# Performance work log

Hardware: AMD Instinct MI355X
Metric: run time of the kernel (lower is better)

## Reference

```python
import jax, jax.numpy as jnp
import numpy as np

NUM_HEADS = 32
NUM_KV_HEADS = 8
HEAD_DIM = 128
HIDDEN = 4096
RANK = 8
ALPHA = 16.0
SCALING = ALPHA / RANK
EPS = 1e-8


def dora_linear(x, W, A, B, m):
    # DoRA: W_eff = W + scaling * B @ A; directional component normalized per
    # output row, rescaled by learned magnitude m.
    W_eff = W + SCALING * (B @ A)                      # [out, in]
    norm = jnp.linalg.norm(W_eff, axis=1)              # [out]
    W_d = W_eff * (m / (norm + EPS))[:, None]
    return x @ W_d.T


def setup_inputs() -> dict:
    key = jax.random.key(0)
    ks = jax.random.split(key, 16)
    B_, S = 2, 2048
    hidden_states = jax.random.normal(ks[0], (B_, S, HIDDEN), jnp.float32)
    # additive causal mask
    causal = jnp.triu(jnp.full((S, S), -1e9, jnp.float32), k=1)
    attention_mask = jnp.broadcast_to(causal, (B_, 1, S, S))

    def w(k, shape, scale=0.02):
        return scale * jax.random.normal(k, shape, jnp.float32)

    Wq = w(ks[1], (HIDDEN, HIDDEN)); Aq = w(ks[2], (RANK, HIDDEN)); Bq = w(ks[3], (HIDDEN, RANK))
    Wk = w(ks[4], (NUM_KV_HEADS * HEAD_DIM, HIDDEN)); Ak = w(ks[5], (RANK, HIDDEN)); Bk = w(ks[6], (NUM_KV_HEADS * HEAD_DIM, RANK))
    Wv = w(ks[7], (NUM_KV_HEADS * HEAD_DIM, HIDDEN)); Av = w(ks[8], (RANK, HIDDEN)); Bv = w(ks[9], (NUM_KV_HEADS * HEAD_DIM, RANK))
    Wo = w(ks[10], (HIDDEN, HIDDEN)); Ao = w(ks[11], (RANK, HIDDEN)); Bo = w(ks[12], (HIDDEN, RANK))
    # DoRA magnitude init: column-norm of base weight (per output row)
    mq = jnp.linalg.norm(Wq, axis=1)
    mk = jnp.linalg.norm(Wk, axis=1)
    mv = jnp.linalg.norm(Wv, axis=1)
    mo = jnp.linalg.norm(Wo, axis=1)
    return dict(hidden_states=hidden_states, attention_mask=attention_mask,
                Wq=Wq, Aq=Aq, Bq=Bq, mq=mq,
                Wk=Wk, Ak=Ak, Bk=Bk, mk=mk,
                Wv=Wv, Av=Av, Bv=Bv, mv=mv,
                Wo=Wo, Ao=Ao, Bo=Bo, mo=mo)


def reference(hidden_states, attention_mask,
              Wq, Aq, Bq, mq, Wk, Ak, Bk, mk,
              Wv, Av, Bv, mv, Wo, Ao, Bo, mo):
    bsz, q_len, _ = hidden_states.shape
    n_rep = NUM_HEADS // NUM_KV_HEADS

    q = dora_linear(hidden_states, Wq, Aq, Bq, mq)
    k = dora_linear(hidden_states, Wk, Ak, Bk, mk)
    v = dora_linear(hidden_states, Wv, Av, Bv, mv)

    q = q.reshape(bsz, q_len, NUM_HEADS, HEAD_DIM).transpose(0, 2, 1, 3)
    k = k.reshape(bsz, q_len, NUM_KV_HEADS, HEAD_DIM).transpose(0, 2, 1, 3)
    v = v.reshape(bsz, q_len, NUM_KV_HEADS, HEAD_DIM).transpose(0, 2, 1, 3)

    # _apply_rotary_pos_emb is a no-op in the source: (q, k) unchanged

    # repeat_kv for grouped-query attention
    k = jnp.repeat(k, n_rep, axis=1)  # [b, H, s, d]
    v = jnp.repeat(v, n_rep, axis=1)

    scale = 1.0 / jnp.sqrt(jnp.float32(HEAD_DIM))
    attn_weights = jnp.einsum('bhqd,bhkd->bhqk', q, k) * scale
    attn_weights = attn_weights + attention_mask
    attn_weights = jax.nn.softmax(attn_weights, axis=-1)
    attn_output = jnp.einsum('bhqk,bhkd->bhqd', attn_weights, v)
    attn_output = attn_output.transpose(0, 2, 1, 3).reshape(bsz, q_len, HIDDEN)
    attn_output = dora_linear(attn_output, Wo, Ao, Bo, mo)
    return attn_output
```

## Files before the change

### kernel.cpp

```cpp
#include <hip/hip_runtime.h>
#include <hip/hip_bf16.h>
#include <stdint.h>

#define HIDDEN 4096
#define RANK   8
#define SCALING 2.0f
#define EPS    1e-8f
#define SEQ    2048
#define BATCH  2
#define NH     32
#define NKVH   8
#define HD     128
#define MROWS  (BATCH*SEQ)
#define NQKV   6144

typedef __attribute__((ext_vector_type(8))) short bf16x8;
typedef __attribute__((ext_vector_type(4))) short bf16x4;
typedef __attribute__((ext_vector_type(4))) float f32x4;

__device__ __forceinline__ void gload_lds16(const void* g, void* lds) {
  __builtin_amdgcn_global_load_lds((__attribute__((address_space(1))) void*)g,
                                   (__attribute__((address_space(3))) void*)lds,
                                   16, 0, 0);
}

__device__ __forceinline__ unsigned short f2bf(float f) {
  __hip_bfloat16 h = __float2bfloat16(f);
  return *reinterpret_cast<unsigned short*>(&h);
}

__device__ __forceinline__ void store_c(float* p, float v) { *p = v; }
__device__ __forceinline__ void store_c(__hip_bfloat16* p, float v) { *p = __float2bfloat16(v); }

__device__ __forceinline__ bf16x8 lds_read8_b64(const short* p) {
  bf16x4 lo = *(const bf16x4*)p;
  bf16x4 hi = *(const bf16x4*)(p + 4);
  bf16x8 r;
  r[0]=lo[0]; r[1]=lo[1]; r[2]=lo[2]; r[3]=lo[3];
  r[4]=hi[0]; r[5]=hi[1]; r[6]=hi[2]; r[7]=hi[3];
  return r;
}

__device__ __forceinline__ void wd_row(const float* __restrict__ W, const float* __restrict__ A,
                                       const float* __restrict__ B, const float* __restrict__ m,
                                       unsigned short* __restrict__ out, int row, int tid,
                                       float* wsum) {
  float bl[RANK];
#pragma unroll
  for (int t = 0; t < RANK; ++t) bl[t] = SCALING * B[row*RANK + t];
  float ev[16];
  float ss = 0.f;
#pragma unroll
  for (int it = 0; it < 4; ++it) {
    const int j = it*1024 + tid*4;
    const float4 wv = *(const float4*)&W[(size_t)row*HIDDEN + j];
    float e0 = wv.x, e1 = wv.y, e2 = wv.z, e3 = wv.w;
#pragma unroll
    for (int t = 0; t < RANK; ++t) {
      const float4 av = *(const float4*)&A[t*HIDDEN + j];
      e0 += bl[t]*av.x; e1 += bl[t]*av.y; e2 += bl[t]*av.z; e3 += bl[t]*av.w;
    }
    ev[it*4+0]=e0; ev[it*4+1]=e1; ev[it*4+2]=e2; ev[it*4+3]=e3;
    ss += e0*e0 + e1*e1 + e2*e2 + e3*e3;
  }
#pragma unroll
  for (int off = 32; off > 0; off >>= 1) ss += __shfl_down(ss, off, 64);
  if ((tid & 63) == 0) wsum[tid >> 6] = ss;
  __syncthreads();
  const float norm = sqrtf(wsum[0]+wsum[1]+wsum[2]+wsum[3]);
  const float scl = m[row] / (norm + EPS);
#pragma unroll
  for (int it = 0; it < 4; ++it) {
    const int j = it*1024 + tid*4;
    ushort4 pk;
    pk.x = f2bf(ev[it*4+0]*scl); pk.y = f2bf(ev[it*4+1]*scl);
    pk.z = f2bf(ev[it*4+2]*scl); pk.w = f2bf(ev[it*4+3]*scl);
    *(ushort4*)&out[(size_t)row*HIDDEN + j] = pk;
  }
}

__launch_bounds__(256)
__global__ void prep_kernel(const float* __restrict__ x, unsigned short* __restrict__ xbf,
                            const float* Wq, const float* Aq, const float* Bq, const float* mq, unsigned short* wdq,
                            const float* Wk, const float* Ak, const float* Bk, const float* mk, unsigned short* wdk,
                            const float* Wv, const float* Av, const float* Bv, const float* mv, unsigned short* wdv,
                            const float* Wo, const float* Ao, const float* Bo, const float* mo, unsigned short* wdo) {
  __shared__ float wsum[4];
  const int bid = blockIdx.x;
  const int tid = threadIdx.x;
  if (bid < 16384) {
    const size_t i = ((size_t)bid * 256 + tid) * 4;
    const float4 v = *(const float4*)&x[i];
    ushort4 pk;
    pk.x = f2bf(v.x); pk.y = f2bf(v.y); pk.z = f2bf(v.z); pk.w = f2bf(v.w);
    *(ushort4*)&xbf[i] = pk;
  } else if (bid < 20480) {
    wd_row(Wq, Aq, Bq, mq, wdq, bid - 16384, tid, wsum);
  } else if (bid < 21504) {
    wd_row(Wk, Ak, Bk, mk, wdk, bid - 20480, tid, wsum);
  } else if (bid < 22528) {
    wd_row(Wv, Av, Bv, mv, wdv, bid - 21504, tid, wsum);
  } else {
    wd_row(Wo, Ao, Bo, mo, wdo, bid - 22528, tid, wsum);
  }
}

__launch_bounds__(256)
__global__ void wd_kernel(const float* __restrict__ W, const float* __restrict__ A,
                          const float* __restrict__ B, const float* __restrict__ m,
                          unsigned short* __restrict__ out) {
  __shared__ float wsum[4];
  wd_row(W, A, B, m, out, blockIdx.x, threadIdx.x, wsum);
}

__device__ __forceinline__ void stage_unit(const __hip_bfloat16* __restrict__ Ab,
                                           const __hip_bfloat16* __restrict__ Bb,
                                           const int K, __hip_bfloat16* sbuf,
                                           const int tau, const int j,
                                           const int w, const int l, const int kchunk) {
  const __hip_bfloat16* src = (j & 1) ? Bb : Ab;
  __hip_bfloat16* dst = sbuf + ((tau & 1) << 15) + (j << 13);
  const int k0 = (tau << 6) + ((j >> 1) << 5) + (kchunk << 3);
  const int r0 = (w << 4) + (l >> 2);
  gload_lds16(src + (size_t)r0 * K + k0, dst + (w << 9));
  gload_lds16(src + (size_t)(r0 + 128) * K + k0, dst + 4096 + (w << 9));
}

template<typename CT, int NREP>
__launch_bounds__(512, 2)
__global__ void gemm256(const __hip_bfloat16* __restrict__ A,
                        const __hip_bfloat16* __restrict__ B,
                        CT* __restrict__ C, const int M, const int N, const int K) {
  (void)M;
  __shared__ __hip_bfloat16 sb[65536];
  const int tid = threadIdx.x;
  const int w = tid >> 6, l = tid & 63;
  const int wr = w >> 2, wc = w & 3;
  const int q4 = l >> 4, ln = l & 15;
  const int nbn = N / (NREP * 64);
  const int cpx = gridDim.x >> 3;
  const int fid = (blockIdx.x & 7) * cpx + (blockIdx.x >> 3);
  const int tM = (fid / nbn) << 8;
  const int tN = (fid % nbn) * (NREP * 64);
  const int NT = K >> 6;
  const __hip_bfloat16* Ab = A + (size_t)tM * K;
  const __hip_bfloat16* Bb = B + (size_t)tN * K;
  const int kchunk = (l & 3) ^ ((l >> 3) & 3);
  const int slotoff = (q4 ^ ((ln >> 1) & 3)) << 3;

  f32x4 acc[8][NREP] = {};
  bf16x8 bfr[NREP] = {};

#pragma unroll
  for (int s = 0; s < 6; ++s)
    stage_unit(Ab, Bb, K, sb, s >> 2, s & 3, w, l, kchunk);
  asm volatile("s_waitcnt vmcnt(4)" ::: "memory");
  __builtin_amdgcn_s_barrier();

  for (int tt = 0; tt < NT; tt += 2) {
#pragma unroll
    for (int hlf = 0; hlf < 2; ++hlf) {
      const int t_ = tt + hlf;
      const short* base = (const short*)sb + (hlf << 15);
#pragma unroll
      for (int q = 0; q < 4; ++q) {
        const int ks = q >> 1;
        const int mh = q & 1;
        bf16x8 af[4];
        const short* Au = base + (ks << 14);
#pragma unroll
        for (int i = 0; i < 4; ++i) {
          const int row = wr * 128 + (mh * 4 + i) * 16 + ln;
          af[i] = *(const bf16x8*)&Au[row * 32 + slotoff];
        }
        if (mh == 0) {
          const short* Bu = base + 8192 + (ks << 14);
#pragma unroll
          for (int i = 0; i < NREP; ++i) {
            const int row = wc * (NREP * 16) + i * 16 + ln;
            bfr[i] = *(const bf16x8*)&Bu[row * 32 + slotoff];
          }
        }
        const int s = 4 * t_ + 6 + q;
        if ((s >> 2) < NT)
          stage_unit(Ab, Bb, K, sb, s >> 2, s & 3, w, l, kchunk);
        __builtin_amdgcn_s_barrier();
        __builtin_amdgcn_s_setprio(1);
#pragma unroll
        for (int i = 0; i < 4; ++i)
#pragma unroll
          for (int ni = 0; ni < NREP; ++ni)
            acc[mh * 4 + i][ni] = __builtin_amdgcn_mfma_f32_16x16x32_bf16(af[i], bfr[ni], acc[mh * 4 + i][ni], 0, 0, 0);
        __builtin_amdgcn_s_setprio(0);
        if (q == 3 && t_ < NT - 1) {
          if (t_ == NT - 2) asm volatile("s_waitcnt vmcnt(0)" ::: "memory");
          else              asm volatile("s_waitcnt vmcnt(4)" ::: "memory");
        }
        __builtin_amdgcn_s_barrier();
      }
    }
  }

  const int r0 = tM + wr * 128 + q4 * 4;
  const int c0 = tN + wc * (NREP * 16) + ln;
#pragma unroll
  for (int mi = 0; mi < 8; ++mi)
#pragma unroll
    for (int ni = 0; ni < NREP; ++ni)
#pragma unroll
      for (int r = 0; r < 4; ++r)
        store_c(&C[(size_t)(r0 + mi * 16 + r) * N + c0 + ni * 16], acc[mi][ni][r]);
}

#define VT_S 68
#define PS_S 68
__launch_bounds__(256, 3)
__global__ void attn_kernel(const __hip_bfloat16* __restrict__ qkv,
                            __hip_bfloat16* __restrict__ out) {
  const int bid = blockIdx.x;
  const int qt = 15 - (bid >> 6);
  const int hb = bid & 63;
  const int h  = hb & 31;
  const int b  = hb >> 5;
  const int kvh = h >> 2;
  const int tid = threadIdx.x;
  const int w = tid >> 6, l = tid & 63;
  const int q4 = l >> 4;
  const int ln = l & 15;
  const int sw = ln & 7;

  __shared__ __hip_bfloat16 Ks[64*128];
  __shared__ __hip_bfloat16 Vt[128*VT_S];
  __shared__ __hip_bfloat16 Ps[4][2][16*PS_S];

  const __hip_bfloat16* kb = qkv + (size_t)(b*SEQ)*NQKV + HIDDEN + kvh*HD;
  const __hip_bfloat16* vb = qkv + (size_t)(b*SEQ)*NQKV + (HIDDEN+1024) + kvh*HD;

  const int Q0 = qt*128;

  const int krow = l >> 4;
  const int kchunk = ((l & 15) ^ krow ^ ((w & 1) << 2)) * 8;

  const int vc4 = (tid & 15) * 4;
  const int vd0 = (tid >> 4) * 8;

  bf16x8 aq[2][4];
#pragma unroll
  for (int hf = 0; hf < 2; ++hf) {
    const __hip_bfloat16* qr = qkv + (size_t)(b*SEQ + Q0 + hf*64 + w*16 + ln)*NQKV + h*HD;
#pragma unroll
    for (int ks = 0; ks < 4; ++ks) {
      uint4 raw = *(const uint4*)(qr + ks*32 + q4*8);
      aq[hf][ks] = *(const bf16x8*)&raw;
    }
  }

  f32x4 o[2][8] = {};
  float mx[2] = {-1e30f, -1e30f};
  float lsum[2] = {0.f, 0.f};
  const float sc = 0.08838834764831845f;
  const int qabs0 = Q0 + w*16 + ln;

  const int jmax = 2*qt + 1;
  for (int j = 0; j <= jmax; ++j) {
    const int do0 = (j <= 2*qt);
    __syncthreads();
#pragma unroll
    for (int i = 0; i < 4; ++i) {
      const int rr = i*16 + w*4;
      gload_lds16(kb + (size_t)(j*64 + rr + krow)*NQKV + kchunk, &Ks[rr*128]);
    }
    {
      uint4 r0 = *(const uint4*)(vb + (size_t)(j*64 + vc4 + 0)*NQKV + vd0);
      uint4 r1 = *(const uint4*)(vb + (size_t)(j*64 + vc4 + 1)*NQKV + vd0);
      uint4 r2 = *(const uint4*)(vb + (size_t)(j*64 + vc4 + 2)*NQKV + vd0);
      uint4 r3 = *(const uint4*)(vb + (size_t)(j*64 + vc4 + 3)*NQKV + vd0);
      const unsigned short* p0 = (const unsigned short*)&r0;
      const unsigned short* p1 = (const unsigned short*)&r1;
      const unsigned short* p2 = (const unsigned short*)&r2;
      const unsigned short* p3 = (const unsigned short*)&r3;
#pragma unroll
      for (int t = 0; t < 8; ++t) {
        ushort4 pk; pk.x = p0[t]; pk.y = p1[t]; pk.z = p2[t]; pk.w = p3[t];
        *(ushort4*)&Vt[(vd0 + t)*VT_S + vc4] = pk;
      }
    }
    __syncthreads();

    f32x4 s[2][4] = {};
    const short* Kp = (const short*)Ks;
#pragma unroll
    for (int ks = 0; ks < 4; ++ks) {
      const int slot = ((ks*4 + q4) ^ sw) * 8;
#pragma unroll
      for (int nt = 0; nt < 4; ++nt) {
        bf16x8 bk = *(const bf16x8*)&Kp[(nt*16 + ln)*128 + slot];
        if (do0) s[0][nt] = __builtin_amdgcn_mfma_f32_16x16x32_bf16(bk, aq[0][ks], s[0][nt], 0, 0, 0);
        s[1][nt] = __builtin_amdgcn_mfma_f32_16x16x32_bf16(bk, aq[1][ks], s[1][nt], 0, 0, 0);
      }
    }

#pragma unroll
    for (int hf = 0; hf < 2; ++hf) {
      if (hf == 0 && !do0) continue;
      const int qabs = qabs0 + hf*64;
      if (j == 2*qt + hf) {
#pragma unroll
        for (int nt = 0; nt < 4; ++nt)
#pragma unroll
          for (int r = 0; r < 4; ++r) {
            const int kvabs = j*64 + nt*16 + q4*4 + r;
            if (kvabs > qabs) s[hf][nt][r] = -1e30f;
          }
      }
      float vmax = mx[hf];
#pragma unroll
      for (int nt = 0; nt < 4; ++nt)
#pragma unroll
        for (int r = 0; r < 4; ++r) vmax = fmaxf(vmax, s[hf][nt][r]);
      vmax = fmaxf(vmax, __shfl_xor(vmax, 16, 64));
      vmax = fmaxf(vmax, __shfl_xor(vmax, 32, 64));
      const float alpha = __expf((mx[hf] - vmax) * sc);
      float rs = 0.f;
#pragma unroll
      for (int nt = 0; nt < 4; ++nt)
#pragma unroll
        for (int r = 0; r < 4; ++r) {
          const float e = __expf((s[hf][nt][r] - vmax) * sc);
          s[hf][nt][r] = e; rs += e;
        }
      rs += __shfl_xor(rs, 16, 64);
      rs += __shfl_xor(rs, 32, 64);
      mx[hf] = vmax;
      lsum[hf] = lsum[hf]*alpha + rs;
#pragma unroll
      for (int r = 0; r < 4; ++r) {
        const float ar = __shfl(alpha, q4*4 + r, 64);
#pragma unroll
        for (int ni = 0; ni < 8; ++ni) o[hf][ni][r] *= ar;
      }
      __hip_bfloat16* Pw = Ps[w][hf];
#pragma unroll
      for (int nt = 0; nt < 4; ++nt) {
        ushort4 pk;
        pk.x = f2bf(s[hf][nt][0]); pk.y = f2bf(s[hf][nt][1]);
        pk.z = f2bf(s[hf][nt][2]); pk.w = f2bf(s[hf][nt][3]);
        *(ushort4*)&Pw[ln*PS_S + nt*16 + q4*4] = pk;
      }
    }

    const short* Vp = (const short*)Vt;
    const short* Pp0 = (const short*)Ps[w][0];
    const short* Pp1 = (const short*)Ps[w][1];
#pragma unroll
    for (int ks = 0; ks < 2; ++ks) {
      bf16x8 ap0 = lds_read8_b64(&Pp0[ln*PS_S + ks*32 + q4*8]);
      bf16x8 ap1 = lds_read8_b64(&Pp1[ln*PS_S + ks*32 + q4*8]);
#pragma unroll
      for (int ni = 0; ni < 8; ++ni) {
        bf16x8 bv = lds_read8_b64(&Vp[(ni*16 + ln)*VT_S + ks*32 + q4*8]);
        if (do0) o[0][ni] = __builtin_amdgcn_mfma_f32_16x16x32_bf16(ap0, bv, o[0][ni], 0, 0, 0);
        o[1][ni] = __builtin_amdgcn_mfma_f32_16x16x32_bf16(ap1, bv, o[1][ni], 0, 0, 0);
      }
    }
  }

#pragma unroll
  for (int hf = 0; hf < 2; ++hf) {
    const int row0 = b*SEQ + Q0 + hf*64 + w*16 + q4*4;
#pragma unroll
    for (int r = 0; r < 4; ++r) {
      const float lr = __shfl(lsum[hf], q4*4 + r, 64);
      const float inv = 1.f / lr;
#pragma unroll
      for (int ni = 0; ni < 8; ++ni)
        out[(size_t)(row0 + r)*HIDDEN + h*HD + ni*16 + ln] = __float2bfloat16(o[hf][ni][r] * inv);
    }
  }
}

extern "C" void kernel_launch(void* const* d_in, const int* in_sizes, int n_in,
                              void* d_out, int out_size, void* d_ws, size_t ws_size,
                              hipStream_t stream) {
  (void)in_sizes; (void)n_in; (void)out_size;
  const float* x  = (const float*)d_in[0];
  const float* Wq = (const float*)d_in[2];
  const float* Aq = (const float*)d_in[3];
  const float* Bq = (const float*)d_in[4];
  const float* mq = (const float*)d_in[5];
  const float* Wk = (const float*)d_in[6];
  const float* Ak = (const float*)d_in[7];
  const float* Bk = (const float*)d_in[8];
  const float* mk = (const float*)d_in[9];
  const float* Wv = (const float*)d_in[10];
  const float* Av = (const float*)d_in[11];
  const float* Bv = (const float*)d_in[12];
  const float* mv = (const float*)d_in[13];
  const float* Wo = (const float*)d_in[14];
  const float* Ao = (const float*)d_in[15];
  const float* Bo = (const float*)d_in[16];
  const float* mo = (const float*)d_in[17];

  char* ws = (char*)d_ws;
  __hip_bfloat16* xbf = (__hip_bfloat16*)ws;
  __hip_bfloat16* wd  = (__hip_bfloat16*)(ws + (size_t)33554432);
  __hip_bfloat16* qkv = (__hip_bfloat16*)(ws + (size_t)83886080);
  const bool big = ws_size >= (size_t)167772160;
  __hip_bfloat16* wdo = big ? (__hip_bfloat16*)(ws + (size_t)134217728) : wd;

  prep_kernel<<<big ? 26624 : 22528, 256, 0, stream>>>(
      x, (unsigned short*)xbf,
      Wq, Aq, Bq, mq, (unsigned short*)wd,
      Wk, Ak, Bk, mk, (unsigned short*)(wd + (size_t)4096*4096),
      Wv, Av, Bv, mv, (unsigned short*)(wd + (size_t)5120*4096),
      Wo, Ao, Bo, mo, (unsigned short*)wdo);
  gemm256<__hip_bfloat16, 3><<<512, 512, 0, stream>>>(xbf, wd, qkv, MROWS, NQKV, HIDDEN);
  if (!big)
    wd_kernel<<<4096, 256, 0, stream>>>(Wo, Ao, Bo, mo, (unsigned short*)wdo);
  attn_kernel<<<1024, 256, 0, stream>>>(qkv, xbf);
  gemm256<float, 4><<<256, 512, 0, stream>>>(xbf, wdo, (float*)d_out, MROWS, HIDDEN, HIDDEN);
}
```

Measured before the change: 791.1 us.

## Software-pipeline GEMM LDS fragment loads with register double-buffering and fewer barriers

Restructures the gemm256 main loop so the A/B fragments for the next MFMA phase are read from LDS into a second register set while the current phase's MFMAs are issued. The two barriers per phase become one, and the global-to-LDS staging and vmcnt waits are re-timed to match (an explicit buffer parity parameter, wait counts of 8 and 6). The aim is to hide LDS read latency behind MFMA work and cut synchronisation stalls. The cost is higher register pressure from the doubled fragment arrays, and the changed wait counts add a risk of LDS read/write hazards.

New measurement: 781.9 us. Within noise of the previous version (-1.2%).

```diff
diff --git a/kernel.cpp b/kernel.cpp
--- a/kernel.cpp
+++ b/kernel.cpp
@@ -113,13 +113,13 @@
   wd_row(W, A, B, m, out, blockIdx.x, threadIdx.x, wsum);
 }
 
-__device__ __forceinline__ void stage_unit(const __hip_bfloat16* __restrict__ Ab,
-                                           const __hip_bfloat16* __restrict__ Bb,
-                                           const int K, __hip_bfloat16* sbuf,
-                                           const int tau, const int j,
-                                           const int w, const int l, const int kchunk) {
+__device__ __forceinline__ void stage_u(const __hip_bfloat16* __restrict__ Ab,
+                                        const __hip_bfloat16* __restrict__ Bb,
+                                        const int K, __hip_bfloat16* sbuf,
+                                        const int par, const int tau, const int j,
+                                        const int w, const int l, const int kchunk) {
   const __hip_bfloat16* src = (j & 1) ? Bb : Ab;
-  __hip_bfloat16* dst = sbuf + ((tau & 1) << 15) + (j << 13);
+  __hip_bfloat16* dst = sbuf + (par << 15) + (j << 13);
   const int k0 = (tau << 6) + ((j >> 1) << 5) + (kchunk << 3);
   const int r0 = (w << 4) + (l >> 2);
   gload_lds16(src + (size_t)r0 * K + k0, dst + (w << 9));
@@ -149,55 +149,58 @@
   const int slotoff = (q4 ^ ((ln >> 1) & 3)) << 3;
 
   f32x4 acc[8][NREP] = {};
-  bf16x8 bfr[NREP] = {};
+  bf16x8 af[2][4];
+  bf16x8 bfr[2][NREP];
+  const short* sp = (const short*)sb;
+  const int arow0 = wr * 128 + ln;
+  const int brow0 = wc * (NREP * 16) + ln;
 
 #pragma unroll
   for (int s = 0; s < 6; ++s)
-    stage_unit(Ab, Bb, K, sb, s >> 2, s & 3, w, l, kchunk);
-  asm volatile("s_waitcnt vmcnt(4)" ::: "memory");
+    stage_u(Ab, Bb, K, sb, (s >> 2) & 1, s >> 2, s & 3, w, l, kchunk);
+  asm volatile("s_waitcnt vmcnt(8)" ::: "memory");
   __builtin_amdgcn_s_barrier();
+#pragma unroll
+  for (int i = 0; i < 4; ++i)
+    af[0][i] = *(const bf16x8*)&sp[(arow0 + i*16) * 32 + slotoff];
+#pragma unroll
+  for (int i = 0; i < NREP; ++i)
+    bfr[0][i] = *(const bf16x8*)&sp[8192 + (brow0 + i*16) * 32 + slotoff];
 
   for (int tt = 0; tt < NT; tt += 2) {
 #pragma unroll
-    for (int hlf = 0; hlf < 2; ++hlf) {
-      const int t_ = tt + hlf;
-      const short* base = (const short*)sb + (hlf << 15);
-#pragma unroll
-      for (int q = 0; q < 4; ++q) {
-        const int ks = q >> 1;
-        const int mh = q & 1;
-        bf16x8 af[4];
-        const short* Au = base + (ks << 14);
-#pragma unroll
-        for (int i = 0; i < 4; ++i) {
-          const int row = wr * 128 + (mh * 4 + i) * 16 + ln;
-          af[i] = *(const bf16x8*)&Au[row * 32 + slotoff];
+    for (int pp = 0; pp < 8; ++pp) {
+      const int q = pp & 3, ks = q >> 1, mh = q & 1;
+      __builtin_amdgcn_s_setprio(1);
+#pragma unroll
+      for (int i = 0; i < 4; ++i)
+#pragma unroll
+        for (int ni = 0; ni < NREP; ++ni)
+          acc[mh*4 + i][ni] = __builtin_amdgcn_mfma_f32_16x16x32_bf16(af[pp & 1][i], bfr[ks][ni], acc[mh*4+i][ni], 0, 0, 0);
+      __builtin_amdgcn_s_setprio(0);
+      {
+        const int pn = pp + 1;
+        const int nb  = ((pn >> 2) & 1) << 15;
+        const int nks = (pn & 3) >> 1;
+        const int nmh = pn & 1;
+#pragma unroll
+        for (int i = 0; i < 4; ++i)
+          af[pn & 1][i] = *(const bf16x8*)&sp[nb + (nks << 14) + (arow0 + (nmh*4+i)*16) * 32 + slotoff];
+        if ((pn & 1) == 0) {
+#pragma unroll
+          for (int i = 0; i < NREP; ++i)
+            bfr[nks][i] = *(const bf16x8*)&sp[nb + 8192 + (nks << 14) + (brow0 + i*16) * 32 + slotoff];
         }
-        if (mh == 0) {
-          const short* Bu = base + 8192 + (ks << 14);
-#pragma unroll
-          for (int i = 0; i < NREP; ++i) {
-            const int row = wc * (NREP * 16) + i * 16 + ln;
-            bfr[i] = *(const bf16x8*)&Bu[row * 32 + slotoff];
-          }
-        }
-        const int s = 4 * t_ + 6 + q;
-        if ((s >> 2) < NT)
-          stage_unit(Ab, Bb, K, sb, s >> 2, s & 3, w, l, kchunk);
-        __builtin_amdgcn_s_barrier();
-        __builtin_amdgcn_s_setprio(1);
-#pragma unroll
-        for (int i = 0; i < 4; ++i)
-#pragma unroll
-          for (int ni = 0; ni < NREP; ++ni)
-            acc[mh * 4 + i][ni] = __builtin_amdgcn_mfma_f32_16x16x32_bf16(af[i], bfr[ni], acc[mh * 4 + i][ni], 0, 0, 0);
-        __builtin_amdgcn_s_setprio(0);
-        if (q == 3 && t_ < NT - 1) {
-          if (t_ == NT - 2) asm volatile("s_waitcnt vmcnt(0)" ::: "memory");
-          else              asm volatile("s_waitcnt vmcnt(4)" ::: "memory");
-        }
-        __builtin_amdgcn_s_barrier();
-      }
+      }
+      {
+        const int su = pp + 6;
+        const int stau = tt + (su >> 2);
+        if (stau < NT)
+          stage_u(Ab, Bb, K, sb, (su >> 2) & 1, stau, su & 3, w, l, kchunk);
+      }
+      if ((pp & 1) == 0)
+        asm volatile("s_waitcnt vmcnt(6)" ::: "memory");
+      __builtin_amdgcn_s_barrier();
     }
   }
 
```
